# Kernel optimization log

Hardware: AMD Instinct MI355X
Metric: run time of the kernel (lower is better)

## Reference

```python
import jax, jax.numpy as jnp
import numpy as np

CORR_THRESHOLD = 0.5
EPS = 1e-12


def setup_inputs() -> dict:
    key = jax.random.key(0)
    # x: [B, N_channels, T] EEG windows
    x = jax.random.normal(key, (128, 64, 30720), dtype=jnp.float32)
    return {"x": x}


def reference(x):
    # Batched Pearson correlation across channels (rows = variables, like np.corrcoef).
    B, N, T = x.shape
    xc = x - jnp.mean(x, axis=-1, keepdims=True)            # center over time
    cov = jnp.einsum("bnt,bmt->bnm", xc, xc)                # [B, N, N] unnormalized
    norms = jnp.sqrt(jnp.einsum("bnt,bnt->bn", xc, xc))     # [B, N] row L2 norms
    corr = cov / (norms[:, :, None] * norms[:, None, :] + EPS)
    # zero diagonal, then threshold on |corr|
    eye = jnp.eye(N, dtype=bool)
    corr = jnp.where(eye[None], 0.0, corr)
    mask = jnp.abs(corr) >= CORR_THRESHOLD
    adj = jnp.where(mask, corr, 0.0)                        # dense masked adjacency [B, N, N]
    # node features are the raw EEG samples (as in the original Data(x=eeg_sample, ...))
    return adj, x
```

## Files before the change

kernel.cpp:

```cpp
#include <hip/hip_runtime.h>
#include <hip/hip_bf16.h>
#include <cstdint>
#include <cstddef>

#define B_   128
#define NCH  64
#define T_   30720
#define TW   256
#define EPSF 1e-12f
#define THRF 0.5f

typedef float  f32x4 __attribute__((ext_vector_type(4)));
typedef short  s16x8 __attribute__((ext_vector_type(8)));
typedef unsigned short u16;

#define AS1 __attribute__((address_space(1)))
#define AS3 __attribute__((address_space(3)))

static __device__ __forceinline__ short bf16s(float f) {
    return (short)__builtin_bit_cast(u16, __float2bfloat16(f));
}

__global__ __launch_bounds__(1024) void corr_stage1(
    const float* __restrict__ x, float* __restrict__ out_x,
    float* __restrict__ P, float* __restrict__ S,
    int split, int Tc)
{
    extern __shared__ __align__(16) float lds[];

    const int tid  = threadIdx.x;
    const int lane = tid & 63;
    const int w    = tid >> 6;

    const int bid = blockIdx.x;
    const int b   = bid / split;
    const int c   = bid - b * split;

    const size_t base = (size_t)b * ((size_t)NCH * T_) + (size_t)c * Tc;
    const float* xw = x + base;
    float*       ow = out_x + base;

    const int NT  = Tc / TW;
    const int BUF = NCH * TW;

    auto dma = [&](int tile, int buf) {
        #pragma unroll
        for (int i = 0; i < 4; ++i) {
            const int r  = w * 4 + i;
            const int gg = lane ^ (r & 7);
            const float* src = xw + (size_t)r * T_ + (size_t)(tile * TW + gg * 4);
            float* dst = &lds[buf * BUF + r * TW];
            __builtin_amdgcn_global_load_lds((const AS1 void*)src,
                                             (AS3 void*)dst, 16, 0, 0);
        }
    };

    dma(0, 0);
    asm volatile("s_waitcnt vmcnt(0)" ::: "memory");
    __builtin_amdgcn_s_barrier();
    __builtin_amdgcn_sched_barrier(0);

    if (w < 8) {
        float csum[8];
        #pragma unroll
        for (int i = 0; i < 8; ++i) csum[i] = 0.f;

        for (int t = 0; t < NT; ++t) {
            const int cur = t & 1;
            if (t + 1 < NT) dma(t + 1, cur ^ 1);

            #pragma unroll
            for (int i = 0; i < 8; ++i) {
                const int row  = w * 8 + i;
                const int slot = lane ^ (row & 7);
                const f32x4 v = *reinterpret_cast<const f32x4*>(
                    &lds[cur * BUF + row * TW + slot * 4]);
                *reinterpret_cast<f32x4*>(
                    ow + (size_t)row * T_ + (size_t)(t * TW + lane * 4)) = v;
                csum[i] += ((v.x + v.y) + (v.z + v.w));
            }

            asm volatile("s_waitcnt vmcnt(8)" ::: "memory");
            __builtin_amdgcn_s_barrier();
            __builtin_amdgcn_sched_barrier(0);
        }

        __syncthreads();

        #pragma unroll
        for (int i = 0; i < 8; ++i) {
            float v = csum[i];
            v += __shfl_xor(v, 1,  64);
            v += __shfl_xor(v, 2,  64);
            v += __shfl_xor(v, 4,  64);
            v += __shfl_xor(v, 8,  64);
            v += __shfl_xor(v, 16, 64);
            v += __shfl_xor(v, 32, 64);
            if (lane == 0)
                S[(size_t)bid * NCH + w * 8 + i] = v;
        }
    } else {
        const int g   = w - 8;
        const int q   = g & 3;
        const int par = g >> 2;
        const int qr  = q >> 1, qc = q & 1;
        const int fr  = lane & 15;
        const int g8  = lane >> 4;
        const int fs  = fr & 7;

        f32x4 acc[2][2];
        #pragma unroll
        for (int rb = 0; rb < 2; ++rb)
            #pragma unroll
            for (int cb = 0; cb < 2; ++cb) acc[rb][cb] = (f32x4)(0.f);

        for (int t = 0; t < NT; ++t) {
            const int cur = t & 1;
            if (t + 1 < NT) dma(t + 1, cur ^ 1);

            #pragma unroll
            for (int kk = 0; kk < 4; ++kk) {
                const int ks = par + 2 * kk;
                const int gl = (ks * 8 + 2 * g8) ^ fs;
                const int gh = (ks * 8 + 2 * g8 + 1) ^ fs;
                s16x8 frag[4];
                #pragma unroll
                for (int e = 0; e < 4; ++e) {
                    const int blk = (e < 2) ? (2 * qr + e) : (2 * qc + (e - 2));
                    const int ro  = cur * BUF + (blk * 16 + fr) * TW;
                    const f32x4 lo = *reinterpret_cast<const f32x4*>(&lds[ro + gl * 4]);
                    const f32x4 hv = *reinterpret_cast<const f32x4*>(&lds[ro + gh * 4]);
                    frag[e][0] = bf16s(lo.x); frag[e][1] = bf16s(lo.y);
                    frag[e][2] = bf16s(lo.z); frag[e][3] = bf16s(lo.w);
                    frag[e][4] = bf16s(hv.x); frag[e][5] = bf16s(hv.y);
                    frag[e][6] = bf16s(hv.z); frag[e][7] = bf16s(hv.w);
                }
                #pragma unroll
                for (int rb = 0; rb < 2; ++rb)
                    #pragma unroll
                    for (int cb = 0; cb < 2; ++cb)
                        acc[rb][cb] = __builtin_amdgcn_mfma_f32_16x16x32_bf16(
                            frag[rb], frag[2 + cb], acc[rb][cb], 0, 0, 0);
            }

            asm volatile("s_waitcnt vmcnt(0)" ::: "memory");
            __builtin_amdgcn_s_barrier();
            __builtin_amdgcn_sched_barrier(0);
        }

        if (par == 1) {
            #pragma unroll
            for (int rb = 0; rb < 2; ++rb)
                #pragma unroll
                for (int cb = 0; cb < 2; ++cb)
                    #pragma unroll
                    for (int reg = 0; reg < 4; ++reg)
                        lds[q * 1024 + lane * 16 + rb * 8 + cb * 4 + reg]
                            = acc[rb][cb][reg];
        }

        __syncthreads();

        if (par == 0) {
            float* Pc = P + ((size_t)bid << 12);
            const int prow = (lane >> 4) << 2;
            const int pcol = lane & 15;
            #pragma unroll
            for (int rb = 0; rb < 2; ++rb)
                #pragma unroll
                for (int cb = 0; cb < 2; ++cb)
                    #pragma unroll
                    for (int reg = 0; reg < 4; ++reg)
                        Pc[((2 * qr + rb) * 16 + prow + reg) * 64
                           + (2 * qc + cb) * 16 + pcol]
                            = acc[rb][cb][reg]
                            + lds[q * 1024 + lane * 16 + rb * 8 + cb * 4 + reg];
        }
    }
}

__global__ __launch_bounds__(256) void corr_stage2(
    const float* __restrict__ P, const float* __restrict__ S,
    float* __restrict__ adj, int split)
{
    const int idx = blockIdx.x * 256 + threadIdx.x;
    const int b  = idx >> 12;
    const int nm = idx & 4095;
    const int n  = nm >> 6;
    const int m  = nm & 63;

    float G = 0.f, Gnn = 0.f, Gmm = 0.f, Sn = 0.f, Sm = 0.f;
    for (int c = 0; c < split; ++c) {
        const float* Pc = P + ((size_t)(b * split + c) << 12);
        const float* Sc = S + (size_t)(b * split + c) * NCH;
        G   += Pc[nm];
        Gnn += Pc[n * 65];
        Gmm += Pc[m * 65];
        Sn  += Sc[n];
        Sm  += Sc[m];
    }
    const float invT = 1.0f / (float)T_;
    const float cov  = G   - Sn * Sm * invT;
    const float vn   = Gnn - Sn * Sn * invT;
    const float vm   = Gmm - Sm * Sm * invT;
    const float den  = sqrtf(vn) * sqrtf(vm) + EPSF;
    float corr = cov / den;
    if (n == m) corr = 0.f;
    adj[idx] = (fabsf(corr) >= THRF) ? corr : 0.f;
}

extern "C" void kernel_launch(void* const* d_in, const int* in_sizes, int n_in,
                              void* d_out, int out_size, void* d_ws, size_t ws_size,
                              hipStream_t stream)
{
    const float* x   = (const float*)d_in[0];
    float* out   = (float*)d_out;
    float* adj   = out;
    float* out_x = out + (size_t)B_ * NCH * NCH;

    const int split = 2;
    float* P = (float*)d_ws;
    float* S = P + (size_t)B_ * split * 4096;
    const int Tc = T_ / split;

    corr_stage1<<<dim3(B_ * split), dim3(1024), 131072, stream>>>(
        x, out_x, P, S, split, Tc);
    corr_stage2<<<dim3((B_ * 4096) / 256), dim3(256), 0, stream>>>(P, S, adj, split);
}
```

Before: 433.4 us.

## Split raw-sample passthrough copy into a separate kernel from Gram accumulation

Moves the copy of x to the output buffer out of the Gram/sum kernel into a dedicated per-wave double-buffered copy kernel. The Gram kernel no longer issues global stores, so its waits tighten to vmcnt(0). The aim is to stop stores from contending with the MFMA pipeline and DMA waits. The cost is that the input is read from global memory twice and there is an extra kernel launch.

```diff
diff --git a/kernel.cpp b/kernel.cpp
--- a/kernel.cpp
+++ b/kernel.cpp
@@ -21,8 +21,9 @@
     return (short)__builtin_bit_cast(u16, __float2bfloat16(f));
 }
 
-__global__ __launch_bounds__(1024) void corr_stage1(
-    const float* __restrict__ x, float* __restrict__ out_x,
+
+__global__ __launch_bounds__(1024) void corr_gram(
+    const float* __restrict__ x,
     float* __restrict__ P, float* __restrict__ S,
     int split, int Tc)
 {
@@ -38,7 +39,6 @@
 
     const size_t base = (size_t)b * ((size_t)NCH * T_) + (size_t)c * Tc;
     const float* xw = x + base;
-    float*       ow = out_x + base;
 
     const int NT  = Tc / TW;
     const int BUF = NCH * TW;
@@ -75,12 +75,10 @@
                 const int slot = lane ^ (row & 7);
                 const f32x4 v = *reinterpret_cast<const f32x4*>(
                     &lds[cur * BUF + row * TW + slot * 4]);
-                *reinterpret_cast<f32x4*>(
-                    ow + (size_t)row * T_ + (size_t)(t * TW + lane * 4)) = v;
                 csum[i] += ((v.x + v.y) + (v.z + v.w));
             }
 
-            asm volatile("s_waitcnt vmcnt(8)" ::: "memory");
+            asm volatile("s_waitcnt vmcnt(0)" ::: "memory");
             __builtin_amdgcn_s_barrier();
             __builtin_amdgcn_sched_barrier(0);
         }
@@ -175,6 +173,61 @@
                            + (2 * qc + cb) * 16 + pcol]
                             = acc[rb][cb][reg]
                             + lds[q * 1024 + lane * 16 + rb * 8 + cb * 4 + reg];
+        }
+    }
+}
+
+__global__ __launch_bounds__(1024) void corr_copy(
+    const float* __restrict__ x, float* __restrict__ out_x,
+    int split, int Tc)
+{
+    extern __shared__ __align__(16) float ldsc[];
+
+    const int tid  = threadIdx.x;
+    const int lane = tid & 63;
+    const int w    = tid >> 6;
+
+    const int bid = blockIdx.x;
+    const int b   = bid / split;
+    const int c   = bid - b * split;
+
+    const size_t base = (size_t)b * ((size_t)NCH * T_) + (size_t)c * Tc
+                      + (size_t)(w * 4) * T_;
+    const float* xw = x + base;
+    float*       ow = out_x + base;
+
+    const int NT = Tc / TW;
+    float* Lw = &ldsc[w * 2048];
+
+    auto dma = [&](int tile, int buf) {
+        #pragma unroll
+        for (int i = 0; i < 4; ++i) {
+            const float* src = xw + (size_t)i * T_ + (size_t)(tile * TW + lane * 4);
+            float* dst = Lw + buf * 1024 + i * 256;
+            __builtin_amdgcn_global_load_lds((const AS1 void*)src,
+                                             (AS3 void*)dst, 16, 0, 0);
+        }
+    };
+
+    dma(0, 0);
+
+    for (int t = 0; t < NT; ++t) {
+        const int cur = t & 1;
+        if (t + 1 < NT) dma(t + 1, cur ^ 1);
+
+        if (t == 0 || t + 1 == NT) {
+            asm volatile("s_waitcnt vmcnt(4)" ::: "memory");
+        } else {
+            asm volatile("s_waitcnt vmcnt(8)" ::: "memory");
+        }
+        __builtin_amdgcn_sched_barrier(0);
+
+        #pragma unroll
+        for (int i = 0; i < 4; ++i) {
+            const f32x4 v = *reinterpret_cast<const f32x4*>(
+                &Lw[cur * 1024 + i * 256 + lane * 4]);
+            *reinterpret_cast<f32x4*>(
+                ow + (size_t)i * T_ + (size_t)(t * TW + lane * 4)) = v;
         }
     }
 }
@@ -223,7 +276,7 @@
     float* S = P + (size_t)B_ * split * 4096;
     const int Tc = T_ / split;
 
-    corr_stage1<<<dim3(B_ * split), dim3(1024), 131072, stream>>>(
-        x, out_x, P, S, split, Tc);
+    corr_gram<<<dim3(B_ * split), dim3(1024), 131072, stream>>>(x, P, S, split, Tc);
+    corr_copy<<<dim3(B_ * split), dim3(1024), 131072, stream>>>(x, out_x, split, Tc);
     corr_stage2<<<dim3((B_ * 4096) / 256), dim3(256), 0, stream>>>(P, S, adj, split);
 }
```

Result: slower. 592.5 us (+36.7%).

## Producer waves load x via registers and feed LDS for MFMA consumer waves

Applied to the files above, without the earlier changes.

The shared global_load_lds DMA, which all 16 waves issued, is removed. The 8 reduction waves now load tiles into double-buffered registers and copy them to the output. They also write each tile into the swizzled LDS buffer while accumulating row sums. The MFMA waves only read from LDS, synchronised with the producers by matching barriers. The goal is to take memory-issue work and vmcnt stalls off the compute waves and overlap loads more deeply, at the cost of extra LDS stores and more register pressure. The loop count is hardcoded to 60 tiles, and a redundant scalar LDS store remains.

```diff
diff --git a/kernel.cpp b/kernel.cpp
--- a/kernel.cpp
+++ b/kernel.cpp
@@ -14,9 +14,6 @@
 typedef short  s16x8 __attribute__((ext_vector_type(8)));
 typedef unsigned short u16;
 
-#define AS1 __attribute__((address_space(1)))
-#define AS3 __attribute__((address_space(3)))
-
 static __device__ __forceinline__ short bf16s(float f) {
     return (short)__builtin_bit_cast(u16, __float2bfloat16(f));
 }
@@ -43,47 +40,54 @@
     const int NT  = Tc / TW;
     const int BUF = NCH * TW;
 
-    auto dma = [&](int tile, int buf) {
-        #pragma unroll
-        for (int i = 0; i < 4; ++i) {
-            const int r  = w * 4 + i;
-            const int gg = lane ^ (r & 7);
-            const float* src = xw + (size_t)r * T_ + (size_t)(tile * TW + gg * 4);
-            float* dst = &lds[buf * BUF + r * TW];
-            __builtin_amdgcn_global_load_lds((const AS1 void*)src,
-                                             (AS3 void*)dst, 16, 0, 0);
-        }
-    };
-
-    dma(0, 0);
-    asm volatile("s_waitcnt vmcnt(0)" ::: "memory");
-    __builtin_amdgcn_s_barrier();
-    __builtin_amdgcn_sched_barrier(0);
-
     if (w < 8) {
+        const float* xr = xw + (size_t)(w * 8) * T_ + (size_t)(lane * 4);
+        float*       or_ = ow + (size_t)(w * 8) * T_ + (size_t)(lane * 4);
+
         float csum[8];
         #pragma unroll
         for (int i = 0; i < 8; ++i) csum[i] = 0.f;
 
-        for (int t = 0; t < NT; ++t) {
-            const int cur = t & 1;
-            if (t + 1 < NT) dma(t + 1, cur ^ 1);
-
+        f32x4 A[8], Bk[8];
+
+        auto LD = [&](f32x4* bank, int tt) {
+            #pragma unroll
+            for (int i = 0; i < 8; ++i)
+                bank[i] = *reinterpret_cast<const f32x4*>(
+                    xr + (size_t)i * T_ + (size_t)(tt * TW));
+        };
+        auto CONS = [&](f32x4* bank, int tt) {
             #pragma unroll
             for (int i = 0; i < 8; ++i) {
-                const int row  = w * 8 + i;
-                const int slot = lane ^ (row & 7);
-                const f32x4 v = *reinterpret_cast<const f32x4*>(
-                    &lds[cur * BUF + row * TW + slot * 4]);
+                const f32x4 v = bank[i];
+                *reinterpret_cast<f32x4*>(or_ + (size_t)i * T_ + (size_t)(tt * TW)) = v;
+                lds[(tt & 1) * BUF + (w * 8 + i) * TW + ((lane ^ i) << 2)] = v.x;
                 *reinterpret_cast<f32x4*>(
-                    ow + (size_t)row * T_ + (size_t)(t * TW + lane * 4)) = v;
+                    &lds[(tt & 1) * BUF + (w * 8 + i) * TW + ((lane ^ i) << 2)]) = v;
                 csum[i] += ((v.x + v.y) + (v.z + v.w));
             }
-
-            asm volatile("s_waitcnt vmcnt(8)" ::: "memory");
-            __builtin_amdgcn_s_barrier();
-            __builtin_amdgcn_sched_barrier(0);
-        }
+        };
+        #define CBAR() do { \
+            asm volatile("s_waitcnt lgkmcnt(0)" ::: "memory"); \
+            __builtin_amdgcn_s_barrier(); \
+            __builtin_amdgcn_sched_barrier(0); } while (0)
+
+        LD(A, 0);
+        LD(Bk, 1);
+        asm volatile("s_waitcnt vmcnt(8)" ::: "memory");
+        CONS(A, 0);  CBAR();
+        for (int t = 1; t <= 57; t += 2) {
+            LD(A, t + 1);
+            asm volatile("s_waitcnt vmcnt(16)" ::: "memory");
+            CONS(Bk, t);  CBAR();
+            LD(Bk, t + 2);
+            asm volatile("s_waitcnt vmcnt(16)" ::: "memory");
+            CONS(A, t + 1);  CBAR();
+        }
+        asm volatile("s_waitcnt vmcnt(8)" ::: "memory");
+        CONS(Bk, 59);  CBAR();
+        CBAR();
+        #undef CBAR
 
         __syncthreads();
 
@@ -114,10 +118,13 @@
             #pragma unroll
             for (int cb = 0; cb < 2; ++cb) acc[rb][cb] = (f32x4)(0.f);
 
+        #define GBAR() do { \
+            __builtin_amdgcn_s_barrier(); \
+            __builtin_amdgcn_sched_barrier(0); } while (0)
+
+        GBAR();
         for (int t = 0; t < NT; ++t) {
             const int cur = t & 1;
-            if (t + 1 < NT) dma(t + 1, cur ^ 1);
-
             #pragma unroll
             for (int kk = 0; kk < 4; ++kk) {
                 const int ks = par + 2 * kk;
@@ -142,11 +149,9 @@
                         acc[rb][cb] = __builtin_amdgcn_mfma_f32_16x16x32_bf16(
                             frag[rb], frag[2 + cb], acc[rb][cb], 0, 0, 0);
             }
-
-            asm volatile("s_waitcnt vmcnt(0)" ::: "memory");
-            __builtin_amdgcn_s_barrier();
-            __builtin_amdgcn_sched_barrier(0);
-        }
+            GBAR();
+        }
+        #undef GBAR
 
         if (par == 1) {
             #pragma unroll
```

New measurement: 450.7 us. 1.04x slower.
